# Kernel optimization log

Hardware: AMD Instinct MI355X
Metric: run time of the kernel (lower is better)

## Reference

```python
import jax, jax.numpy as jnp
import numpy as np

EPS = 1e-20
V, E, H = 32000, 256, 512
SRC_LEN, TGT_LEN, B = 400, 100, 32
PAD, SOS = 0, 1


def setup_inputs() -> dict:
    key = jax.random.key(0)
    ks = jax.random.split(key, 16)
    s = 0.08
    # tokens in [2, V) to avoid PAD/SOS collisions
    source_tensor = jax.random.randint(ks[0], (SRC_LEN, B), 2, V)
    target_tensor = jax.random.randint(ks[1], (TGT_LEN, B), 2, V)
    embedding = jax.random.normal(ks[2], (V, E), jnp.float32) * s
    embedding = embedding.at[PAD].set(0.0)  # padding_idx row zeroed
    return {
        "source_tensor": source_tensor,
        "target_tensor": target_tensor,
        "embedding": embedding,
        "enc_W_ih": jax.random.normal(ks[3], (3 * H, E), jnp.float32) * s,
        "enc_W_hh": jax.random.normal(ks[4], (3 * H, H), jnp.float32) * s,
        "enc_b_ih": jax.random.normal(ks[5], (3 * H,), jnp.float32) * s,
        "enc_b_hh": jax.random.normal(ks[6], (3 * H,), jnp.float32) * s,
        "dec_W_ih": jax.random.normal(ks[7], (3 * H, E), jnp.float32) * s,
        "dec_W_hh": jax.random.normal(ks[8], (3 * H, H), jnp.float32) * s,
        "dec_b_ih": jax.random.normal(ks[9], (3 * H,), jnp.float32) * s,
        "dec_b_hh": jax.random.normal(ks[10], (3 * H,), jnp.float32) * s,
        "pre_W": jax.random.normal(ks[11], (E, H), jnp.float32) * s,
        "pre_b": jax.random.normal(ks[12], (E,), jnp.float32) * s,
        "out_b": jax.random.normal(ks[13], (V,), jnp.float32) * s,
    }


def _gru_cell(x, h, W_ih, W_hh, b_ih, b_hh):
    # PyTorch GRU gate order: [r, z, n]
    gi = x @ W_ih.T + b_ih          # (B, 3H)
    gh = h @ W_hh.T + b_hh          # (B, 3H)
    gi_r, gi_z, gi_n = jnp.split(gi, 3, axis=1)
    gh_r, gh_z, gh_n = jnp.split(gh, 3, axis=1)
    r = jax.nn.sigmoid(gi_r + gh_r)
    z = jax.nn.sigmoid(gi_z + gh_z)
    n = jnp.tanh(gi_n + r * gh_n)
    return (1.0 - z) * n + z * h


def reference(source_tensor, target_tensor, embedding,
              enc_W_ih, enc_W_hh, enc_b_ih, enc_b_hh,
              dec_W_ih, dec_W_hh, dec_b_ih, dec_b_hh,
              pre_W, pre_b, out_b):
    # ---- encoder: GRU over source ----
    src_emb = embedding[source_tensor]                  # (S, B, E)
    h0 = jnp.zeros((B, H), embedding.dtype)

    def enc_step(h, x):
        h = _gru_cell(x, h, enc_W_ih, enc_W_hh, enc_b_ih, enc_b_hh)
        return h, None

    enc_h, _ = jax.lax.scan(enc_step, h0, src_emb)

    # ---- decoder with teacher forcing ----
    sos = jnp.full((1, B), SOS, dtype=source_tensor.dtype)
    dec_inputs = jnp.concatenate([sos, target_tensor[:-1]], axis=0)  # (T, B)

    def dec_step(h, inp):
        tok, gold = inp
        x = embedding[tok]                               # (B, E)
        h = _gru_cell(x, h, dec_W_ih, dec_W_hh, dec_b_ih, dec_b_hh)
        out_emb = h @ pre_W.T + pre_b                    # (B, E)
        logits = out_emb @ embedding.T + out_b           # (B, V) tied weights
        probs = jax.nn.softmax(logits, axis=1)
        top = jnp.argmax(probs, axis=1)
        logp = jnp.log(probs + EPS)
        nll = -jnp.take_along_axis(logp, gold[:, None], axis=1)[:, 0]
        mask = (gold != PAD).astype(logp.dtype)
        loss = jnp.sum(nll * mask) / jnp.maximum(jnp.sum(mask), 1.0)
        return h, (top, loss)

    _, (tokens, losses) = jax.lax.scan(dec_step, enc_h, (dec_inputs, target_tensor))
    total_loss = jnp.sum(losses)
    return tokens, total_loss
```

## Files before the change

kernel.cpp:

```cpp
#include <hip/hip_runtime.h>
#include <hip/hip_cooperative_groups.h>
#include <math.h>

#define VV 32000
#define EE 256
#define HH 512
#define SS 400
#define TT 100
#define BB 32
#define NBLK 128

#define WS_HPP   0u
#define WS_ARR   32768u
#define WS_HALL  288768u
#define WS_OE    (288768u + 1638400u)
#define WS_M     (WS_OE + 819200u)
#define WS_ZZ    (WS_M + 400000u)
#define WS_AM    (WS_ZZ + 400000u)
#define WS_GOLD  (WS_AM + 400000u)
#define WS_NLL   (WS_GOLD + 3200u)

__global__ __launch_bounds__(256) void k_zero(float* p, int n) {
    int i = blockIdx.x * 256 + threadIdx.x;
    if (i < n) p[i] = 0.f;
}

__device__ __forceinline__ float dot4(float4 a, float4 b) {
    return a.x * b.x + a.y * b.y + a.z * b.z + a.w * b.w;
}

__device__ __forceinline__ float4 ld4_coh(const float* p) {
    const unsigned long long* q = (const unsigned long long*)p;
    unsigned long long a = __hip_atomic_load(q + 0, __ATOMIC_RELAXED, __HIP_MEMORY_SCOPE_AGENT);
    unsigned long long b = __hip_atomic_load(q + 1, __ATOMIC_RELAXED, __HIP_MEMORY_SCOPE_AGENT);
    float4 v;
    v.x = __uint_as_float((unsigned)(a & 0xffffffffull));
    v.y = __uint_as_float((unsigned)(a >> 32));
    v.z = __uint_as_float((unsigned)(b & 0xffffffffull));
    v.w = __uint_as_float((unsigned)(b >> 32));
    return v;
}

__device__ __forceinline__ void gi_compute(
    const float* __restrict__ emb, const int* __restrict__ src, const int* __restrict__ tgt,
    int phase, int snext, const float4* __restrict__ Ws4,
    float (*gi_buf)[3][4][4], int w, int bq, int b0)
{
    float acc[3][4][4];
    #pragma unroll
    for (int g = 0; g < 3; ++g)
        #pragma unroll
        for (int c = 0; c < 4; ++c)
            #pragma unroll
            for (int i = 0; i < 4; ++i) acc[g][c][i] = 0.f;
    float4 x0[4], x1[4];
    #pragma unroll
    for (int i = 0; i < 4; ++i) {
        int tk = phase ? (snext ? tgt[(snext - 1) * BB + b0 + i] : 1) : src[snext * BB + b0 + i];
        const float* xr = emb + (size_t)tk * EE + w * 4;
        x0[i] = *(const float4*)xr;
        x1[i] = *(const float4*)(xr + 128);
    }
    #pragma unroll
    for (int g = 0; g < 3; ++g)
        #pragma unroll
        for (int c = 0; c < 4; ++c) {
            float4 w0 = Ws4[(g * 4 + c) * 193 + w];
            float4 w1 = Ws4[(g * 4 + c) * 193 + w + 32];
            #pragma unroll
            for (int i = 0; i < 4; ++i)
                acc[g][c][i] += dot4(x0[i], w0) + dot4(x1[i], w1);
        }
    #pragma unroll
    for (int m = 1; m <= 16; m <<= 1)
        #pragma unroll
        for (int g = 0; g < 3; ++g)
            #pragma unroll
            for (int c = 0; c < 4; ++c)
                #pragma unroll
                for (int i = 0; i < 4; ++i)
                    acc[g][c][i] += __shfl_xor(acc[g][c][i], m);
    if (w == 0)
        #pragma unroll
        for (int g = 0; g < 3; ++g)
            #pragma unroll
            for (int c = 0; c < 4; ++c)
                *(float4*)&gi_buf[bq][g][c][0] =
                    make_float4(acc[g][c][0], acc[g][c][1], acc[g][c][2], acc[g][c][3]);
}

__global__ __launch_bounds__(256, 1) void k_rec5(
    const float* __restrict__ emb, const int* __restrict__ src, const int* __restrict__ tgt,
    const float* __restrict__ eWih, const float* __restrict__ eWhh,
    const float* __restrict__ ebih, const float* __restrict__ ebhh,
    const float* __restrict__ dWih, const float* __restrict__ dWhh,
    const float* __restrict__ dbih, const float* __restrict__ dbhh,
    float* __restrict__ hpp, float* __restrict__ Hall, int* __restrict__ arr)
{
    __shared__ float4 Ws4[12 * 193];
    __shared__ __align__(16) float gi_buf[8][3][4][4];
    __shared__ __align__(16) float gh_buf[8][3][4][4];
    const int tid = threadIdx.x;
    const int w   = tid & 31;
    const int bq  = tid >> 5;
    const int b0  = bq * 4;
    const int cg0 = blockIdx.x * 4;
    const int myline = (blockIdx.x & 7) * 64;

    int s = 0;
    for (int phase = 0; phase < 2; ++phase) {
        const float* Wih = phase ? dWih : eWih;
        const float* Whh = phase ? dWhh : eWhh;
        const float* bih = phase ? dbih : ebih;
        const float* bhh = phase ? dbhh : ebhh;

        for (int u = tid; u < 12 * 192; u += 256) {
            int r = u / 192, q = u - r * 192;
            int g = r >> 2, c = r & 3;
            size_t row = (size_t)(g * HH + cg0 + c);
            float4 v;
            if (q < 64) v = *(const float4*)(Wih + row * EE + q * 4);
            else        v = *(const float4*)(Whh + row * HH + (q - 64) * 4);
            Ws4[r * 193 + q] = v;
        }
        float br_ = 0.f, bz_ = 0.f, bnx_ = 0.f, bnh_ = 0.f;
        if (tid < 128) {
            int cg = cg0 + (tid & 3);
            br_  = bih[cg] + bhh[cg];
            bz_  = bih[HH + cg] + bhh[HH + cg];
            bnx_ = bih[2 * HH + cg];
            bnh_ = bhh[2 * HH + cg];
        }
        __syncthreads();

        gi_compute(emb, src, tgt, phase, 0, Ws4, gi_buf, w, bq, b0);
        __syncthreads();

        const int T = phase ? TT : SS;
        for (int t = 0; t < T; ++t, ++s) {
            const float* hprev; float* hnext;
            if (phase == 0) {
                hprev = hpp + (t & 1) * (BB * HH);
                hnext = hpp + ((t + 1) & 1) * (BB * HH);
            } else {
                hprev = t ? (Hall + (size_t)(t - 1) * (BB * HH)) : hpp;
                hnext = Hall + (size_t)t * (BB * HH);
            }

            float4 hf[4][4];
            #pragma unroll
            for (int i = 0; i < 4; ++i) {
                const float* hr = hprev + (b0 + i) * HH + w * 4;
                #pragma unroll
                for (int jh = 0; jh < 4; ++jh) hf[i][jh] = ld4_coh(hr + jh * 128);
            }
            float ah[3][4][4];
            #pragma unroll
            for (int g = 0; g < 3; ++g)
                #pragma unroll
                for (int c = 0; c < 4; ++c)
                    #pragma unroll
                    for (int i = 0; i < 4; ++i) ah[g][c][i] = 0.f;
            #pragma unroll
            for (int jh = 0; jh < 4; ++jh)
                #pragma unroll
                for (int g = 0; g < 3; ++g)
                    #pragma unroll
                    for (int c = 0; c < 4; ++c) {
                        float4 wv = Ws4[(g * 4 + c) * 193 + 64 + w + 32 * jh];
                        #pragma unroll
                        for (int i = 0; i < 4; ++i)
                            ah[g][c][i] += dot4(hf[i][jh], wv);
                    }
            #pragma unroll
            for (int m = 1; m <= 16; m <<= 1)
                #pragma unroll
                for (int g = 0; g < 3; ++g)
                    #pragma unroll
                    for (int c = 0; c < 4; ++c)
                        #pragma unroll
                        for (int i = 0; i < 4; ++i)
                            ah[g][c][i] += __shfl_xor(ah[g][c][i], m);
            if (w == 0)
                #pragma unroll
                for (int g = 0; g < 3; ++g)
                    #pragma unroll
                    for (int c = 0; c < 4; ++c)
                        *(float4*)&gh_buf[bq][g][c][0] =
                            make_float4(ah[g][c][0], ah[g][c][1], ah[g][c][2], ah[g][c][3]);
            __syncthreads();

            if (tid < 128) {
                int b = tid >> 2, c = tid & 3;
                int bq2 = b >> 2, i2 = b & 3;
                float gr  = gi_buf[bq2][0][c][i2] + gh_buf[bq2][0][c][i2] + br_;
                float gz  = gi_buf[bq2][1][c][i2] + gh_buf[bq2][1][c][i2] + bz_;
                float gnx = gi_buf[bq2][2][c][i2] + bnx_;
                float gnh = gh_buf[bq2][2][c][i2] + bnh_;
                float r = 1.f / (1.f + expf(-gr));
                float z = 1.f / (1.f + expf(-gz));
                float n = tanhf(gnx + r * gnh);
                float hp = __hip_atomic_load(hprev + b * HH + cg0 + c,
                                             __ATOMIC_RELAXED, __HIP_MEMORY_SCOPE_AGENT);
                __hip_atomic_store(hnext + b * HH + cg0 + c, (1.f - z) * n + z * hp,
                                   __ATOMIC_RELAXED, __HIP_MEMORY_SCOPE_AGENT);
            }
            __builtin_amdgcn_s_waitcnt(0);
            __syncthreads();

            if (tid == 0)
                __hip_atomic_fetch_add(arr + (size_t)s * 512 + myline, 1,
                                       __ATOMIC_RELAXED, __HIP_MEMORY_SCOPE_AGENT);

            if (t < T - 1)
                gi_compute(emb, src, tgt, phase, t + 1, Ws4, gi_buf, w, bq, b0);

            if (tid < 64) {
                const int* base = arr + (size_t)s * 512;
                for (;;) {
                    int v = 0;
                    if (tid < 8)
                        v = __hip_atomic_load(base + tid * 64,
                                              __ATOMIC_RELAXED, __HIP_MEMORY_SCOPE_AGENT);
                    v += __shfl_xor(v, 1);
                    v += __shfl_xor(v, 2);
                    v += __shfl_xor(v, 4);
                    if (__shfl(v, 0) == NBLK) break;
                    __builtin_amdgcn_s_sleep(1);
                }
            }
            __syncthreads();
        }
    }
}

__device__ __forceinline__ void gru_step_body(
    const float* __restrict__ emb, const int* __restrict__ tok, int sos,
    const float* __restrict__ Wih, const float* __restrict__ Whh,
    const float* __restrict__ bih, const float* __restrict__ bhh,
    const float* __restrict__ h_in, float* __restrict__ h_out,
    float (*z)[772], float (*part)[3][16][16],
    int tid, int cblk, int bg0)
{
    #pragma unroll
    for (int i = 0; i < 4; ++i) {
        int idx = tid + i * 768;
        if (idx < 1024) {
            int bl = idx >> 6, k4 = idx & 63;
            int tk = sos ? 1 : tok[bg0 + bl];
            *(float4*)&z[bl][k4 * 4] = *(const float4*)(emb + (size_t)tk * EE + k4 * 4);
        } else {
            int j = idx - 1024;
            int bl = j >> 7, k4 = j & 127;
            *(float4*)&z[bl][256 + k4 * 4] = *(const float4*)(h_in + (bg0 + bl) * HH + k4 * 4);
        }
    }
    __syncthreads();
    const int b  = tid & 15;
    const int c  = (tid >> 4) & 15;
    const int kp = tid >> 8;
    const int cg = cblk * 16 + c;
    const float *w0, *w1, *w2; int koff;
    if (kp == 0) {
        w0 = Wih + (size_t)(0 * HH + cg) * EE;
        w1 = Wih + (size_t)(1 * HH + cg) * EE;
        w2 = Wih + (size_t)(2 * HH + cg) * EE;
        koff = 0;
    } else {
        int o = (kp == 1) ? 0 : 256;
        w0 = Whh + (size_t)(0 * HH + cg) * HH + o;
        w1 = Whh + (size_t)(1 * HH + cg) * HH + o;
        w2 = Whh + (size_t)(2 * HH + cg) * HH + o;
        koff = 256 + o;
    }
    float a0 = 0.f, a1 = 0.f, a2 = 0.f;
    #pragma unroll 8
    for (int k4 = 0; k4 < 64; ++k4) {
        float4 zv = *(const float4*)&z[b][koff + k4 * 4];
        float4 v0 = *(const float4*)(w0 + k4 * 4);
        float4 v1 = *(const float4*)(w1 + k4 * 4);
        float4 v2 = *(const float4*)(w2 + k4 * 4);
        a0 += zv.x * v0.x + zv.y * v0.y + zv.z * v0.z + zv.w * v0.w;
        a1 += zv.x * v1.x + zv.y * v1.y + zv.z * v1.z + zv.w * v1.w;
        a2 += zv.x * v2.x + zv.y * v2.y + zv.z * v2.z + zv.w * v2.w;
    }
    part[kp][0][c][b] = a0;
    part[kp][1][c][b] = a1;
    part[kp][2][c][b] = a2;
    __syncthreads();
    if (kp == 0) {
        float gr  = part[0][0][c][b] + part[1][0][c][b] + part[2][0][c][b];
        float gz  = part[0][1][c][b] + part[1][1][c][b] + part[2][1][c][b];
        float gin = part[0][2][c][b];
        float ghn = part[1][2][c][b] + part[2][2][c][b];
        float r  = 1.f / (1.f + expf(-(gr + bih[cg] + bhh[cg])));
        float zg = 1.f / (1.f + expf(-(gz + bih[HH + cg] + bhh[HH + cg])));
        float n  = tanhf(gin + bih[2 * HH + cg] + r * (ghn + bhh[2 * HH + cg]));
        float hp = z[b][256 + cg];
        h_out[(bg0 + b) * HH + cg] = (1.f - zg) * n + zg * hp;
    }
}

__global__ __launch_bounds__(768) void k_gru(
    const float* __restrict__ emb, const int* __restrict__ tok, int sos,
    const float* __restrict__ Wih, const float* __restrict__ Whh,
    const float* __restrict__ bih, const float* __restrict__ bhh,
    const float* __restrict__ h_in, float* __restrict__ h_out)
{
    __shared__ float z[16][772];
    __shared__ float part[3][3][16][16];
    gru_step_body(emb, tok, sos, Wih, Whh, bih, bhh, h_in, h_out,
                  z, part, threadIdx.x, blockIdx.x & 31, (blockIdx.x >> 5) * 16);
}

__global__ __launch_bounds__(256) void k_outemb(
    const float* __restrict__ Hall, const float* __restrict__ preW,
    const float* __restrict__ preb, float* __restrict__ OE)
{
    __shared__ float hs[16][516];
    const int tid = threadIdx.x;
    const int c0 = blockIdx.x * 64;
    const int r0 = blockIdx.y * 16;
    #pragma unroll
    for (int i = 0; i < 8; ++i) {
        int idx = tid + i * 256;
        int rr = idx >> 7, k4 = idx & 127;
        *(float4*)&hs[rr][k4 * 4] = *(const float4*)(Hall + (size_t)(r0 + rr) * HH + k4 * 4);
    }
    __syncthreads();
    const int rr = tid & 15, cc = tid >> 4;
    int cj[4]; float acc[4];
    #pragma unroll
    for (int j = 0; j < 4; ++j) { cj[j] = c0 + cc + 16 * j; acc[j] = preb[cj[j]]; }
    for (int k4 = 0; k4 < 128; ++k4) {
        float4 hv = *(const float4*)&hs[rr][k4 * 4];
        #pragma unroll
        for (int j = 0; j < 4; ++j) {
            float4 wv = *(const float4*)(preW + (size_t)cj[j] * HH + k4 * 4);
            acc[j] += hv.x * wv.x + hv.y * wv.y + hv.z * wv.z + hv.w * wv.w;
        }
    }
    #pragma unroll
    for (int j = 0; j < 4; ++j) OE[(size_t)(r0 + rr) * EE + cj[j]] = acc[j];
}

__global__ __launch_bounds__(256) void k_logits(
    const float* __restrict__ OE, const float* __restrict__ emb,
    const float* __restrict__ outb, const int* __restrict__ tgt,
    float* __restrict__ m_arr, float* __restrict__ z_arr,
    unsigned int* __restrict__ am_arr, float* __restrict__ gold_arr)
{
    __shared__ float oes[64][20];
    __shared__ float ems[256][18];
    const int tid = threadIdx.x;
    const int c0 = blockIdx.x * 256;
    const int r0 = blockIdx.y * 64;
    const int rr  = tid >> 5;
    const int ccg = tid & 31;

    float acc[8][8];
    #pragma unroll
    for (int i = 0; i < 8; ++i)
        #pragma unroll
        for (int j = 0; j < 8; ++j) acc[i][j] = 0.f;

    for (int kc = 0; kc < 16; ++kc) {
        __syncthreads();
        {
            int row = tid >> 2, f4 = tid & 3;
            *(float4*)&oes[row][f4 * 4] =
                *(const float4*)(OE + (size_t)(r0 + row) * EE + kc * 16 + f4 * 4);
        }
        #pragma unroll
        for (int i = 0; i < 8; ++i) {
            int idx = tid + i * 256;
            int col = idx >> 3, f2 = idx & 7;
            *(float2*)&ems[col][f2 * 2] =
                *(const float2*)(emb + (size_t)(c0 + col) * EE + kc * 16 + f2 * 2);
        }
        __syncthreads();
        #pragma unroll
        for (int kk = 0; kk < 16; kk += 4) {
            float4 ov[8];
            #pragma unroll
            for (int i = 0; i < 8; ++i) ov[i] = *(const float4*)&oes[rr * 8 + i][kk];
            #pragma unroll
            for (int j = 0; j < 8; ++j) {
                float2 e0 = *(const float2*)&ems[ccg + 32 * j][kk];
                float2 e1 = *(const float2*)&ems[ccg + 32 * j][kk + 2];
                #pragma unroll
                for (int i = 0; i < 8; ++i)
                    acc[i][j] += ov[i].x * e0.x + ov[i].y * e0.y + ov[i].z * e1.x + ov[i].w * e1.y;
            }
        }
    }

    #pragma unroll
    for (int i = 0; i < 8; ++i) {
        int r = r0 + rr * 8 + i;
        int gold = tgt[r];
        float vals[8]; float m = -3.4e38f; int cb = 0x7fffffff;
        #pragma unroll
        for (int j = 0; j < 8; ++j) {
            int cj = c0 + ccg + 32 * j;
            float v = acc[i][j] + outb[cj];
            vals[j] = v;
            if (v > m) { m = v; cb = cj; }
            if (cj == gold) gold_arr[r] = v;
        }
        for (int mk = 1; mk <= 16; mk <<= 1) {
            float mo = __shfl_xor(m, mk);
            int   co = __shfl_xor(cb, mk);
            if (mo > m || (mo == m && co < cb)) { m = mo; cb = co; }
        }
        float s = 0.f;
        #pragma unroll
        for (int j = 0; j < 8; ++j) s += expf(vals[j] - m);
        for (int mk = 1; mk <= 16; mk <<= 1) s += __shfl_xor(s, mk);
        if (ccg == 0) {
            size_t p = (size_t)blockIdx.x * 3200 + r;
            m_arr[p] = m; z_arr[p] = s; am_arr[p] = (unsigned)cb;
        }
    }
}

__global__ __launch_bounds__(256) void k_merge(
    const float* __restrict__ m_arr, const float* __restrict__ z_arr,
    const unsigned* __restrict__ am_arr, const float* __restrict__ gold_arr,
    float* __restrict__ nll, float* __restrict__ out)
{
    int r = blockIdx.x * 256 + threadIdx.x;
    if (r >= 3200) return;
    float M = -3.4e38f, Z = 0.f, bm = -3.4e38f; unsigned bc = 0u;
    for (int s = 0; s < 125; ++s) {
        size_t p = (size_t)s * 3200 + r;
        float ms = m_arr[p]; float zs = z_arr[p]; unsigned cs = am_arr[p];
        if (ms > M) { Z = Z * expf(M - ms) + zs; M = ms; }
        else        { Z += zs * expf(ms - M); }
        if (ms > bm || (ms == bm && cs < bc)) { bm = ms; bc = cs; }
    }
    float pg = expf(gold_arr[r] - M) / Z;
    nll[r] = -logf(pg + 1e-20f);
    out[r] = (float)bc;
}

__global__ __launch_bounds__(128) void k_loss(
    const float* __restrict__ nll, const int* __restrict__ tgt, float* __restrict__ out)
{
    __shared__ float ls[128];
    int t = threadIdx.x;
    float lt = 0.f;
    if (t < TT) {
        float s = 0.f; int cnt = 0;
        for (int b = 0; b < BB; ++b) {
            int g = tgt[t * BB + b];
            if (g != 0) { s += nll[t * BB + b]; cnt++; }
        }
        lt = s / fmaxf((float)cnt, 1.f);
    }
    ls[t] = lt;
    __syncthreads();
    for (int off = 64; off > 0; off >>= 1) {
        if (t < off) ls[t] += ls[t + off];
        __syncthreads();
    }
    if (t == 0) out[3200] = ls[0];
}

extern "C" void kernel_launch(void* const* d_in, const int* in_sizes, int n_in,
                              void* d_out, int out_size, void* d_ws, size_t ws_size,
                              hipStream_t stream) {
    const int*   src  = (const int*)  d_in[0];
    const int*   tgt  = (const int*)  d_in[1];
    const float* emb  = (const float*)d_in[2];
    const float* eWih = (const float*)d_in[3];
    const float* eWhh = (const float*)d_in[4];
    const float* ebih = (const float*)d_in[5];
    const float* ebhh = (const float*)d_in[6];
    const float* dWih = (const float*)d_in[7];
    const float* dWhh = (const float*)d_in[8];
    const float* dbih = (const float*)d_in[9];
    const float* dbhh = (const float*)d_in[10];
    const float* preW = (const float*)d_in[11];
    const float* preb = (const float*)d_in[12];
    const float* outb = (const float*)d_in[13];

    float* ws   = (float*)d_ws;
    float* out  = (float*)d_out;
    float* hpp  = ws + WS_HPP;
    int*   arr  = (int*)(ws + WS_ARR);
    float* Hall = ws + WS_HALL;
    float* OE   = ws + WS_OE;
    float* m_a  = ws + WS_M;
    float* z_a  = ws + WS_ZZ;
    unsigned* am_a = (unsigned*)(ws + WS_AM);
    float* gold = ws + WS_GOLD;
    float* nll  = ws + WS_NLL;

    k_zero<<<1128, 256, 0, stream>>>(ws, 288768);

    hipError_t coop_err;
    {
        const float* emb_ = emb; const int* src_ = src; const int* tgt_ = tgt;
        const float* a3 = eWih; const float* a4 = eWhh; const float* a5 = ebih; const float* a6 = ebhh;
        const float* a7 = dWih; const float* a8 = dWhh; const float* a9 = dbih; const float* a10 = dbhh;
        float* hpp_ = hpp; float* Hall_ = Hall; int* arr_ = arr;
        void* args[] = { (void*)&emb_, (void*)&src_, (void*)&tgt_,
                         (void*)&a3, (void*)&a4, (void*)&a5, (void*)&a6,
                         (void*)&a7, (void*)&a8, (void*)&a9, (void*)&a10,
                         (void*)&hpp_, (void*)&Hall_, (void*)&arr_ };
        coop_err = hipLaunchCooperativeKernel((const void*)k_rec5, dim3(NBLK), dim3(256),
                                              args, 0, stream);
    }
    if (coop_err != hipSuccess) {
        for (int t = 0; t < SS; ++t) {
            const float* hin = hpp + (t & 1) * (BB * HH);
            float* hout      = hpp + ((t + 1) & 1) * (BB * HH);
            k_gru<<<64, 768, 0, stream>>>(emb, src + t * BB, 0,
                                          eWih, eWhh, ebih, ebhh, hin, hout);
        }
        for (int t = 0; t < TT; ++t) {
            const float* hin = (t == 0) ? hpp : (Hall + (size_t)(t - 1) * BB * HH);
            float* hout      = Hall + (size_t)t * BB * HH;
            const int* tp    = (t == 0) ? src : (tgt + (t - 1) * BB);
            k_gru<<<64, 768, 0, stream>>>(emb, tp, (t == 0) ? 1 : 0,
                                          dWih, dWhh, dbih, dbhh, hin, hout);
        }
    }

    k_outemb<<<dim3(4, 200), 256, 0, stream>>>(Hall, preW, preb, OE);
    k_logits<<<dim3(125, 50), 256, 0, stream>>>(OE, emb, outb, tgt, m_a, z_a, am_a, gold);
    k_merge<<<13, 256, 0, stream>>>(m_a, z_a, am_a, gold, nll, out);
    k_loss<<<1, 128, 0, stream>>>(nll, tgt, out);
}
```

Before: 7.615 ms.

## Add per-XCD forwarder blocks that copy hidden state into XCD-local buffers

```diff
diff --git a/kernel.cpp b/kernel.cpp
--- a/kernel.cpp
+++ b/kernel.cpp
@@ -12,13 +12,17 @@
 
 #define WS_HPP   0u
 #define WS_ARR   32768u
-#define WS_HALL  288768u
-#define WS_OE    (288768u + 1638400u)
-#define WS_M     (WS_OE + 819200u)
-#define WS_ZZ    (WS_M + 400000u)
-#define WS_AM    (WS_ZZ + 400000u)
-#define WS_GOLD  (WS_AM + 400000u)
-#define WS_NLL   (WS_GOLD + 3200u)
+#define WS_WX    160768u
+#define WS_XF    160832u
+#define WS_INIT  161344u
+#define WS_XB    161408u
+#define WS_HALL  292480u
+#define WS_OE    1930880u
+#define WS_M     2750080u
+#define WS_ZZ    3150080u
+#define WS_AM    3550080u
+#define WS_GOLD  3950080u
+#define WS_NLL   3953280u
 
 __global__ __launch_bounds__(256) void k_zero(float* p, int n) {
     int i = blockIdx.x * 256 + threadIdx.x;
@@ -89,23 +93,126 @@
                     make_float4(acc[g][c][0], acc[g][c][1], acc[g][c][2], acc[g][c][3]);
 }
 
-__global__ __launch_bounds__(256, 1) void k_rec5(
+__global__ __launch_bounds__(256, 1) void k_rec6(
     const float* __restrict__ emb, const int* __restrict__ src, const int* __restrict__ tgt,
     const float* __restrict__ eWih, const float* __restrict__ eWhh,
     const float* __restrict__ ebih, const float* __restrict__ ebhh,
     const float* __restrict__ dWih, const float* __restrict__ dWhh,
     const float* __restrict__ dbih, const float* __restrict__ dbhh,
-    float* __restrict__ hpp, float* __restrict__ Hall, int* __restrict__ arr)
+    float* __restrict__ hpp, float* __restrict__ Hall, int* __restrict__ arr,
+    int* __restrict__ wx, int* __restrict__ xflag, int* __restrict__ initc,
+    float* __restrict__ xbuf)
 {
     __shared__ float4 Ws4[12 * 193];
     __shared__ __align__(16) float gi_buf[8][3][4][4];
     __shared__ __align__(16) float gh_buf[8][3][4][4];
+    __shared__ int oksh, wssh, fastsh;
     const int tid = threadIdx.x;
+    const unsigned myxcd = __builtin_amdgcn_s_getreg(63508) & 0xF;
+
+    if (blockIdx.x < 8) {
+        const int w = blockIdx.x;
+        float* xb = xbuf + (size_t)w * 16384;
+        if (tid == 0) {
+            unsigned long long tA = (unsigned long long)clock64();
+            volatile int* vb = (volatile int*)xb;
+            vb[0] = (int)tA; vb[1] = (int)(tA >> 32);
+            __builtin_amdgcn_s_waitcnt(0);
+            __hip_atomic_store(wx + 8 + 2 * w, (int)tA, __ATOMIC_RELAXED, __HIP_MEMORY_SCOPE_AGENT);
+            __hip_atomic_store(wx + 9 + 2 * w, (int)(tA >> 32), __ATOMIC_RELAXED, __HIP_MEMORY_SCOPE_AGENT);
+            __hip_atomic_store(wx + w, (int)myxcd, __ATOMIC_RELAXED, __HIP_MEMORY_SCOPE_AGENT);
+            __hip_atomic_fetch_add(initc, 1, __ATOMIC_RELAXED, __HIP_MEMORY_SCOPE_AGENT);
+            while (__hip_atomic_load(initc + 16, __ATOMIC_RELAXED, __HIP_MEMORY_SCOPE_AGENT) < NBLK)
+                __builtin_amdgcn_s_sleep(2);
+            unsigned long long tB = tA ^ 0xA5A5A5A55A5A5A5Aull;
+            vb[0] = (int)tB; vb[1] = (int)(tB >> 32);
+            __builtin_amdgcn_s_waitcnt(0);
+            __hip_atomic_store(wx + 24 + 2 * w, (int)tB, __ATOMIC_RELAXED, __HIP_MEMORY_SCOPE_AGENT);
+            __hip_atomic_store(wx + 25 + 2 * w, (int)(tB >> 32), __ATOMIC_RELAXED, __HIP_MEMORY_SCOPE_AGENT);
+            __hip_atomic_fetch_add(initc + 32, 1, __ATOMIC_RELAXED, __HIP_MEMORY_SCOPE_AGENT);
+        }
+        __syncthreads();
+        for (int s = 0; s < 499; ++s) {
+            if (tid < 64) {
+                const int* base = arr + (size_t)s * 256;
+                for (;;) {
+                    int v = 0;
+                    if (tid < 8)
+                        v = __hip_atomic_load(base + tid * 32,
+                                              __ATOMIC_RELAXED, __HIP_MEMORY_SCOPE_AGENT);
+                    v += __shfl_xor(v, 1);
+                    v += __shfl_xor(v, 2);
+                    v += __shfl_xor(v, 4);
+                    if (__shfl(v, 0) == NBLK) break;
+                    __builtin_amdgcn_s_sleep(1);
+                }
+            }
+            __syncthreads();
+            const float* hsrc = (s + 1 <= SS) ? (hpp + (size_t)((s + 1) & 1) * (BB * HH))
+                                              : (Hall + (size_t)(s - SS) * (BB * HH));
+            float4 tmp[16];
+            #pragma unroll
+            for (int k = 0; k < 16; ++k) tmp[k] = ld4_coh(hsrc + tid * 4 + k * 1024);
+            #pragma unroll
+            for (int k = 0; k < 16; ++k) *(float4*)(xb + tid * 4 + k * 1024) = tmp[k];
+            __builtin_amdgcn_s_waitcnt(0);
+            __syncthreads();
+            if (tid == 0) {
+                int fv = s + 1;
+                int* fp = xflag + w * 64;
+                asm volatile("global_store_dword %0, %1, off sc1" :: "v"(fp), "v"(fv) : "memory");
+            }
+        }
+        return;
+    }
+
+    const int p   = blockIdx.x - 8;
     const int w   = tid & 31;
     const int bq  = tid >> 5;
     const int b0  = bq * 4;
-    const int cg0 = blockIdx.x * 4;
-    const int myline = (blockIdx.x & 7) * 64;
+    const int cg0 = p * 4;
+    const int myline = (p & 7) * 32;
+
+    if (tid == 0) {
+        while (__hip_atomic_load(initc, __ATOMIC_RELAXED, __HIP_MEMORY_SCOPE_AGENT) < 8)
+            __builtin_amdgcn_s_sleep(2);
+        int ws_ = -1;
+        for (int ww = 0; ww < 8; ++ww)
+            if (ws_ < 0 &&
+                __hip_atomic_load(wx + ww, __ATOMIC_RELAXED, __HIP_MEMORY_SCOPE_AGENT) == (int)myxcd)
+                ws_ = ww;
+        int okA = 0;
+        if (ws_ >= 0) {
+            const float* vp = xbuf + (size_t)ws_ * 16384;
+            int a, b;
+            asm volatile("global_load_dword %0, %2, off sc0\n\t"
+                         "global_load_dword %1, %2, off offset:4 sc0\n\t"
+                         "s_waitcnt vmcnt(0)"
+                         : "=&v"(a), "=&v"(b) : "v"(vp) : "memory");
+            okA = (a == __hip_atomic_load(wx + 8 + 2 * ws_, __ATOMIC_RELAXED, __HIP_MEMORY_SCOPE_AGENT) &&
+                   b == __hip_atomic_load(wx + 9 + 2 * ws_, __ATOMIC_RELAXED, __HIP_MEMORY_SCOPE_AGENT));
+        }
+        __hip_atomic_fetch_add(initc + 16, 1, __ATOMIC_RELAXED, __HIP_MEMORY_SCOPE_AGENT);
+        while (__hip_atomic_load(initc + 32, __ATOMIC_RELAXED, __HIP_MEMORY_SCOPE_AGENT) < 8)
+            __builtin_amdgcn_s_sleep(2);
+        int okB = 0;
+        if (ws_ >= 0 && okA) {
+            const float* vp = xbuf + (size_t)ws_ * 16384;
+            int a, b;
+            asm volatile("global_load_dword %0, %2, off sc0\n\t"
+                         "global_load_dword %1, %2, off offset:4 sc0\n\t"
+                         "s_waitcnt vmcnt(0)"
+                         : "=&v"(a), "=&v"(b) : "v"(vp) : "memory");
+            okB = (a == __hip_atomic_load(wx + 24 + 2 * ws_, __ATOMIC_RELAXED, __HIP_MEMORY_SCOPE_AGENT) &&
+                   b == __hip_atomic_load(wx + 25 + 2 * ws_, __ATOMIC_RELAXED, __HIP_MEMORY_SCOPE_AGENT));
+        }
+        wssh = ws_;
+        fastsh = (ws_ >= 0) && okA && okB;
+    }
+    __syncthreads();
+    const int  wstar   = wssh;
+    const bool fast_ok = (fastsh != 0);
+    const float* xb = xbuf + (size_t)(wstar < 0 ? 0 : wstar) * 16384;
 
     int s = 0;
     for (int phase = 0; phase < 2; ++phase) {
@@ -132,7 +239,6 @@
             bnh_ = bhh[2 * HH + cg];
         }
         __syncthreads();
-
         gi_compute(emb, src, tgt, phase, 0, Ws4, gi_buf, w, bq, b0);
         __syncthreads();
 
@@ -148,12 +254,82 @@
             }
 
             float4 hf[4][4];
-            #pragma unroll
-            for (int i = 0; i < 4; ++i) {
-                const float* hr = hprev + (b0 + i) * HH + w * 4;
+            if (s == 0) {
                 #pragma unroll
-                for (int jh = 0; jh < 4; ++jh) hf[i][jh] = ld4_coh(hr + jh * 128);
+                for (int i = 0; i < 4; ++i) {
+                    const float* hr = hprev + (b0 + i) * HH + w * 4;
+                    #pragma unroll
+                    for (int jh = 0; jh < 4; ++jh) hf[i][jh] = *(const float4*)(hr + jh * 128);
+                }
+            } else {
+                int ok = 0;
+                if (fast_ok) {
+                    if (tid == 0) {
+                        int o = 0;
+                        for (int it = 0; it < 512; ++it) {
+                            if (__hip_atomic_load(xflag + wstar * 64,
+                                    __ATOMIC_RELAXED, __HIP_MEMORY_SCOPE_AGENT) >= s) { o = 1; break; }
+                            __builtin_amdgcn_s_sleep(1);
+                        }
+                        oksh = o;
+                    }
+                    __syncthreads();
+                    ok = oksh;
+                }
+                if (ok) {
+                    const float* q0 = xb + (b0 + 0) * HH + w * 4;
+                    const float* q1 = xb + (b0 + 1) * HH + w * 4;
+                    const float* q2 = xb + (b0 + 2) * HH + w * 4;
+                    const float* q3 = xb + (b0 + 3) * HH + w * 4;
+                    asm volatile(
+                        "global_load_dwordx4 %0, %16, off sc0\n\t"
+                        "global_load_dwordx4 %1, %16, off offset:512 sc0\n\t"
+                        "global_load_dwordx4 %2, %16, off offset:1024 sc0\n\t"
+                        "global_load_dwordx4 %3, %16, off offset:1536 sc0\n\t"
+                        "global_load_dwordx4 %4, %17, off sc0\n\t"
+                        "global_load_dwordx4 %5, %17, off offset:512 sc0\n\t"
+                        "global_load_dwordx4 %6, %17, off offset:1024 sc0\n\t"
+                        "global_load_dwordx4 %7, %17, off offset:1536 sc0\n\t"
+                        "global_load_dwordx4 %8, %18, off sc0\n\t"
+                        "global_load_dwordx4 %9, %18, off offset:512 sc0\n\t"
+                        "global_load_dwordx4 %10, %18, off offset:1024 sc0\n\t"
+                        "global_load_dwordx4 %11, %18, off offset:1536 sc0\n\t"
+                        "global_load_dwordx4 %12, %19, off sc0\n\t"
+                        "global_load_dwordx4 %13, %19, off offset:512 sc0\n\t"
+                        "global_load_dwordx4 %14, %19, off offset:1024 sc0\n\t"
+                        "global_load_dwordx4 %15, %19, off offset:1536 sc0\n\t"
+                        "s_waitcnt vmcnt(0)"
+                        : "=&v"(hf[0][0]), "=&v"(hf[0][1]), "=&v"(hf[0][2]), "=&v"(hf[0][3]),
+                          "=&v"(hf[1][0]), "=&v"(hf[1][1]), "=&v"(hf[1][2]), "=&v"(hf[1][3]),
+                          "=&v"(hf[2][0]), "=&v"(hf[2][1]), "=&v"(hf[2][2]), "=&v"(hf[2][3]),
+                          "=&v"(hf[3][0]), "=&v"(hf[3][1]), "=&v"(hf[3][2]), "=&v"(hf[3][3])
+                        : "v"(q0), "v"(q1), "v"(q2), "v"(q3)
+                        : "memory");
+                } else {
+                    if (tid < 64) {
+                        const int* base = arr + (size_t)(s - 1) * 256;
+                        for (;;) {
+                            int v = 0;
+                            if (tid < 8)
+                                v = __hip_atomic_load(base + tid * 32,
+                                                      __ATOMIC_RELAXED, __HIP_MEMORY_SCOPE_AGENT);
+                            v += __shfl_xor(v, 1);
+                            v += __shfl_xor(v, 2);
+                            v += __shfl_xor(v, 4);
+                            if (__shfl(v, 0) == NBLK) break;
+                            __builtin_amdgcn_s_sleep(1);
+                        }
+                    }
+                    __syncthreads();
+                    #pragma unroll
+                    for (int i = 0; i < 4; ++i) {
+                        const float* hr = hprev + (b0 + i) * HH + w * 4;
+                        #pragma unroll
+                        for (int jh = 0; jh < 4; ++jh) hf[i][jh] = ld4_coh(hr + jh * 128);
+                    }
+                }
             }
+
             float ah[3][4][4];
             #pragma unroll
             for (int g = 0; g < 3; ++g)
@@ -207,28 +383,11 @@
             }
             __builtin_amdgcn_s_waitcnt(0);
             __syncthreads();
-
             if (tid == 0)
-                __hip_atomic_fetch_add(arr + (size_t)s * 512 + myline, 1,
+                __hip_atomic_fetch_add(arr + (size_t)s * 256 + myline, 1,
                                        __ATOMIC_RELAXED, __HIP_MEMORY_SCOPE_AGENT);
-
             if (t < T - 1)
                 gi_compute(emb, src, tgt, phase, t + 1, Ws4, gi_buf, w, bq, b0);
-
-            if (tid < 64) {
-                const int* base = arr + (size_t)s * 512;
-                for (;;) {
-                    int v = 0;
-                    if (tid < 8)
-                        v = __hip_atomic_load(base + tid * 64,
-                                              __ATOMIC_RELAXED, __HIP_MEMORY_SCOPE_AGENT);
-                    v += __shfl_xor(v, 1);
-                    v += __shfl_xor(v, 2);
-                    v += __shfl_xor(v, 4);
-                    if (__shfl(v, 0) == NBLK) break;
-                    __builtin_amdgcn_s_sleep(1);
-                }
-            }
             __syncthreads();
         }
     }
@@ -489,6 +648,10 @@
     float* out  = (float*)d_out;
     float* hpp  = ws + WS_HPP;
     int*   arr  = (int*)(ws + WS_ARR);
+    int*   wx   = (int*)(ws + WS_WX);
+    int*   xfl  = (int*)(ws + WS_XF);
+    int*   ini  = (int*)(ws + WS_INIT);
+    float* xbuf = ws + WS_XB;
     float* Hall = ws + WS_HALL;
     float* OE   = ws + WS_OE;
     float* m_a  = ws + WS_M;
@@ -497,7 +660,7 @@
     float* gold = ws + WS_GOLD;
     float* nll  = ws + WS_NLL;
 
-    k_zero<<<1128, 256, 0, stream>>>(ws, 288768);
+    k_zero<<<631, 256, 0, stream>>>(ws, 161408);
 
     hipError_t coop_err;
     {
@@ -505,11 +668,13 @@
         const float* a3 = eWih; const float* a4 = eWhh; const float* a5 = ebih; const float* a6 = ebhh;
         const float* a7 = dWih; const float* a8 = dWhh; const float* a9 = dbih; const float* a10 = dbhh;
         float* hpp_ = hpp; float* Hall_ = Hall; int* arr_ = arr;
+        int* wx_ = wx; int* xfl_ = xfl; int* ini_ = ini; float* xbuf_ = xbuf;
         void* args[] = { (void*)&emb_, (void*)&src_, (void*)&tgt_,
                          (void*)&a3, (void*)&a4, (void*)&a5, (void*)&a6,
                          (void*)&a7, (void*)&a8, (void*)&a9, (void*)&a10,
-                         (void*)&hpp_, (void*)&Hall_, (void*)&arr_ };
-        coop_err = hipLaunchCooperativeKernel((const void*)k_rec5, dim3(NBLK), dim3(256),
+                         (void*)&hpp_, (void*)&Hall_, (void*)&arr_,
+                         (void*)&wx_, (void*)&xfl_, (void*)&ini_, (void*)&xbuf_ };
+        coop_err = hipLaunchCooperativeKernel((const void*)k_rec6, dim3(NBLK + 8), dim3(256),
                                               args, 0, stream);
     }
     if (coop_err != hipSuccess) {
```

Result: faster. 7.304 ms (-4.1%).
